# Kernel tuning notes

Hardware: AMD Instinct MI355X
Metric: run time of the kernel (lower is better)

The kernel has to match this reference:

```python
import jax, jax.numpy as jnp
import numpy as np

OUT_F, IN_F, BLOCK, RANK = 8192, 8192, 32, 16
B, S = 4, 256
Q_ZERO = 128.0      # symmetric int8-style zero point for the Q8_0-like quants
LORA_SCALE = 2.0    # patch alpha applied by the patch function


def setup_inputs() -> dict:
    key = jax.random.key(0)
    k1, k2, k3, k4, k5, k6 = jax.random.split(key, 6)
    x = jax.random.normal(k1, (B, S, IN_F), dtype=jnp.float32)
    # block-quantized weight: int quants in [0,256) and per-block scales
    q_int = jax.random.randint(k2, (OUT_F, IN_F // BLOCK, BLOCK), 0, 256, dtype=jnp.int32)
    scales = jax.random.uniform(k3, (OUT_F, IN_F // BLOCK), dtype=jnp.float32) * 0.02
    lora_A = jax.random.normal(k4, (RANK, IN_F), dtype=jnp.float32) * 0.02
    lora_B = jax.random.normal(k5, (OUT_F, RANK), dtype=jnp.float32) * 0.02
    bias = jax.random.normal(k6, (OUT_F,), dtype=jnp.float32)
    return {"x": x, "q_int": q_int, "scales": scales,
            "lora_A": lora_A, "lora_B": lora_B, "bias": bias}


def reference(x, q_int, scales, lora_A, lora_B, bias):
    # --- get_weight(): dequantize GGML block-quantized tensor ---
    # w[o, b, e] = (q[o, b, e] - 128) * scale[o, b]
    w = (q_int.astype(jnp.float32) - Q_ZERO) * scales[:, :, None]   # [out, in//BLOCK, BLOCK]
    w = w.reshape(OUT_F, IN_F)                                      # [out, in]
    # --- apply patch function (LoRA add) ---
    w = w + LORA_SCALE * (lora_B @ lora_A)                          # [out, in]
    # --- cast_bias_weight + F.linear ---
    w = w.astype(x.dtype)
    y = jnp.einsum('bsi,oi->bso', x, w) + bias.astype(x.dtype)      # [B, S, out]
    return y
```

## Files before the change

### kernel.cpp

```cpp
#include <hip/hip_runtime.h>
#include <hip/hip_bf16.h>
#include <stdint.h>

#define OUT_F 8192
#define IN_F  8192
#define RANK  16
#define M_TOT 1024
#define BM 128
#define BN 128
#define BK 64
#define WP 72

typedef __bf16 bf16x8 __attribute__((ext_vector_type(8)));
typedef float  f32x4  __attribute__((ext_vector_type(4)));

static __device__ __forceinline__ uint32_t pack_bf16(float lo, float hi) {
    uint32_t a = __builtin_bit_cast(uint32_t, lo);
    uint32_t b = __builtin_bit_cast(uint32_t, hi);
    return ((a + 0x8000u) >> 16) | ((b + 0x8000u) & 0xffff0000u);
}

__global__ __launch_bounds__(256) void prep_kernel(
    const float* __restrict__ x, const float* __restrict__ lora_A,
    uint2* __restrict__ xb2, float* __restrict__ t)
{
    const int m   = blockIdx.x;
    const int tid = threadIdx.x;
    const float4* x4 = (const float4*)(x + (size_t)m * IN_F);
    uint2* xout = xb2 + (size_t)m * (IN_F / 4);

    float acc[RANK];
#pragma unroll
    for (int r = 0; r < RANK; ++r) acc[r] = 0.f;

#pragma unroll
    for (int j = 0; j < 8; ++j) {
        const int idx4 = tid + 256 * j;
        const float4 v = x4[idx4];
        uint2 p;
        p.x = pack_bf16(v.x, v.y);
        p.y = pack_bf16(v.z, v.w);
        xout[idx4] = p;
        const int i = idx4 * 4;
#pragma unroll
        for (int r = 0; r < RANK; ++r) {
            const float4 a = *(const float4*)(lora_A + (size_t)r * IN_F + i);
            acc[r] += v.x * a.x + v.y * a.y + v.z * a.z + v.w * a.w;
        }
    }
#pragma unroll
    for (int r = 0; r < RANK; ++r) {
        float v = acc[r];
        for (int off = 32; off > 0; off >>= 1) v += __shfl_down(v, off, 64);
        acc[r] = v;
    }
    __shared__ float part[4][RANK];
    const int wave = tid >> 6, lane = tid & 63;
    if (lane == 0) {
#pragma unroll
        for (int r = 0; r < RANK; ++r) part[wave][r] = acc[r];
    }
    __syncthreads();
    if (tid < RANK)
        t[(size_t)m * RANK + tid] = part[0][tid] + part[1][tid] + part[2][tid] + part[3][tid];
}

__global__ __launch_bounds__(256, 2) void gemm_kernel(
    const uint16_t* __restrict__ xb,
    const int*      __restrict__ q,
    const float*    __restrict__ scales,
    const float*    __restrict__ t,
    const float*    __restrict__ loraB,
    const float*    __restrict__ bias,
    float*          __restrict__ out)
{
    __shared__ __align__(16) uint16_t xs[BM * BK];
    __shared__ __align__(16) uint16_t wt[BN * WP];

    const int bx    = blockIdx.x;
    const int mtile = bx >> 6;
    const int ntile = bx & 63;
    const int m0 = mtile * BM;
    const int n0 = ntile * BN;

    const int tid  = threadIdx.x;
    const int wave = tid >> 6;
    const int lane = tid & 63;
    const int wm = wave & 1, wn = wave >> 1;
    const int fr = lane & 15;
    const int fk = (lane >> 4) * 8;
    const int quad = lane >> 4;

    const int qrow_base = tid >> 4;
    const int qcol4     = (tid & 15) * 4;
    const int qhi       = (tid >> 3) & 1;

    f32x4 acc[4][4];
    const f32x4 z = {0.f, 0.f, 0.f, 0.f};
#pragma unroll
    for (int i = 0; i < 4; ++i)
#pragma unroll
        for (int j = 0; j < 4; ++j) acc[i][j] = z;

    {
        if (tid < 128) {
            const int row = tid;
            const float4* tp = (const float4*)(t + (size_t)(m0 + row) * RANK);
            const float4 v0 = tp[0], v1 = tp[1], v2 = tp[2], v3 = tp[3];
            uint32_t* dst = (uint32_t*)(xs + row * BK);
            dst[0] = pack_bf16(v0.x, v0.y); dst[1] = pack_bf16(v0.z, v0.w);
            dst[2] = pack_bf16(v1.x, v1.y); dst[3] = pack_bf16(v1.z, v1.w);
            dst[4] = pack_bf16(v2.x, v2.y); dst[5] = pack_bf16(v2.z, v2.w);
            dst[6] = pack_bf16(v3.x, v3.y); dst[7] = pack_bf16(v3.z, v3.w);
#pragma unroll
            for (int i = 8; i < 16; ++i) dst[i] = 0;
        } else {
            const int row = tid - 128;
            const float4* bp = (const float4*)(loraB + (size_t)(n0 + row) * RANK);
            const float4 v0 = bp[0], v1 = bp[1], v2 = bp[2], v3 = bp[3];
            uint32_t* dst = (uint32_t*)(wt + row * WP);
            dst[0] = pack_bf16(2.f * v0.x, 2.f * v0.y); dst[1] = pack_bf16(2.f * v0.z, 2.f * v0.w);
            dst[2] = pack_bf16(2.f * v1.x, 2.f * v1.y); dst[3] = pack_bf16(2.f * v1.z, 2.f * v1.w);
            dst[4] = pack_bf16(2.f * v2.x, 2.f * v2.y); dst[5] = pack_bf16(2.f * v2.z, 2.f * v2.w);
            dst[6] = pack_bf16(2.f * v3.x, 2.f * v3.y); dst[7] = pack_bf16(2.f * v3.z, 2.f * v3.w);
#pragma unroll
            for (int i = 8; i < 16; ++i) dst[i] = 0;
        }
        __syncthreads();
        bf16x8 af[4], bfr[4];
#pragma unroll
        for (int i = 0; i < 4; ++i)
            af[i] = *(const bf16x8*)(xs + (wm * 64 + i * 16 + fr) * BK + fk);
#pragma unroll
        for (int j = 0; j < 4; ++j)
            bfr[j] = *(const bf16x8*)(wt + (wn * 64 + j * 16 + fr) * WP + fk);
#pragma unroll
        for (int i = 0; i < 4; ++i)
#pragma unroll
            for (int j = 0; j < 4; ++j)
                acc[i][j] = __builtin_amdgcn_mfma_f32_16x16x32_bf16(af[i], bfr[j], acc[i][j], 0, 0, 0);
    }

    const int* qbase = q + (size_t)n0 * IN_F + qcol4;
    const uint16_t* xsrc = xb + (size_t)(m0 + wave * 32 + (lane >> 3)) * IN_F + (lane & 7) * 8;

    for (int kt = 0; kt < IN_F / BK; ++kt) {
        __syncthreads();

        {
            const uint16_t* g = xsrc + kt * BK;
#pragma unroll
            for (int i = 0; i < 4; ++i) {
                __builtin_amdgcn_global_load_lds(
                    (const __attribute__((address_space(1))) uint32_t*)(g + (size_t)i * 8 * IN_F),
                    (__attribute__((address_space(3))) uint32_t*)(xs + (wave * 32 + i * 8) * BK),
                    16, 0, 0);
            }
        }
        {
            int4  qv[8];
            float sc[8];
#pragma unroll
            for (int j = 0; j < 8; ++j) {
                const int row = qrow_base + 16 * j;
                qv[j] = *(const int4*)(qbase + (size_t)row * IN_F + kt * 64);
                sc[j] = scales[(size_t)(n0 + row) * (IN_F / 32) + kt * 2 + qhi];
            }
#pragma unroll
            for (int j = 0; j < 8; ++j) {
                const float s = sc[j];
                const float c = -128.f * s;
                const float f0 = fmaf((float)qv[j].x, s, c);
                const float f1 = fmaf((float)qv[j].y, s, c);
                const float f2 = fmaf((float)qv[j].z, s, c);
                const float f3 = fmaf((float)qv[j].w, s, c);
                uint2 p;
                p.x = pack_bf16(f0, f1);
                p.y = pack_bf16(f2, f3);
                const int row = qrow_base + 16 * j;
                *(uint2*)(wt + row * WP + qcol4) = p;
            }
        }
        __syncthreads();

#pragma unroll
        for (int kk = 0; kk < BK; kk += 32) {
            bf16x8 af[4], bfr[4];
#pragma unroll
            for (int i = 0; i < 4; ++i)
                af[i] = *(const bf16x8*)(xs + (wm * 64 + i * 16 + fr) * BK + kk + fk);
#pragma unroll
            for (int j = 0; j < 4; ++j)
                bfr[j] = *(const bf16x8*)(wt + (wn * 64 + j * 16 + fr) * WP + kk + fk);
#pragma unroll
            for (int i = 0; i < 4; ++i)
#pragma unroll
                for (int j = 0; j < 4; ++j)
                    acc[i][j] = __builtin_amdgcn_mfma_f32_16x16x32_bf16(af[i], bfr[j], acc[i][j], 0, 0, 0);
        }
    }

#pragma unroll
    for (int j = 0; j < 4; ++j) {
        const int col = n0 + wn * 64 + j * 16 + fr;
        const float bv = bias[col];
#pragma unroll
        for (int i = 0; i < 4; ++i) {
            const int rbase = m0 + wm * 64 + i * 16 + quad * 4;
#pragma unroll
            for (int r = 0; r < 4; ++r)
                out[(size_t)(rbase + r) * OUT_F + col] = acc[i][j][r] + bv;
        }
    }
}

extern "C" void kernel_launch(void* const* d_in, const int* in_sizes, int n_in,
                              void* d_out, int out_size, void* d_ws, size_t ws_size,
                              hipStream_t stream) {
    const float* x      = (const float*)d_in[0];
    const int*   q      = (const int*)d_in[1];
    const float* scales = (const float*)d_in[2];
    const float* lora_A = (const float*)d_in[3];
    const float* lora_B = (const float*)d_in[4];
    const float* bias   = (const float*)d_in[5];
    float* out = (float*)d_out;

    uint16_t* xb = (uint16_t*)d_ws;
    float*    t  = (float*)((char*)d_ws + (size_t)M_TOT * IN_F * sizeof(uint16_t));

    prep_kernel<<<M_TOT, 256, 0, stream>>>(x, lora_A, (uint2*)xb, t);
    gemm_kernel<<<(M_TOT / BM) * (OUT_F / BN), 256, 0, stream>>>(
        xb, q, scales, t, lora_B, bias, out);
}
```

Measured before the change: 657.3 us.

## Shrink N tile, prefetch quants across iterations, swizzle LDS, MFMA LoRA projection

Halves the GEMM N tile to 64 and raises the occupancy hint so more blocks fit per CU. The int32 quant and scale loads for the next K step are now issued after the barrier, so they overlap the current MFMA work. The x tile in LDS gets an XOR swizzle to cut bank conflicts. The prep kernel is split into a flat bf16 convert kernel and a separate MFMA-based x·A^T kernel that accumulates with atomics. In exchange, the x tile is reloaded twice as often per output, and the LoRA projection now rounds to bf16 and depends on atomic accumulation order.

```diff
diff --git a/kernel.cpp b/kernel.cpp
--- a/kernel.cpp
+++ b/kernel.cpp
@@ -7,9 +7,10 @@
 #define RANK  16
 #define M_TOT 1024
 #define BM 128
-#define BN 128
+#define BN 64
 #define BK 64
 #define WP 72
+#define NK (IN_F / BK)
 
 typedef __bf16 bf16x8 __attribute__((ext_vector_type(8)));
 typedef float  f32x4  __attribute__((ext_vector_type(4)));
@@ -20,52 +21,61 @@
     return ((a + 0x8000u) >> 16) | ((b + 0x8000u) & 0xffff0000u);
 }
 
-__global__ __launch_bounds__(256) void prep_kernel(
-    const float* __restrict__ x, const float* __restrict__ lora_A,
-    uint2* __restrict__ xb2, float* __restrict__ t)
+__global__ __launch_bounds__(256) void convert_kernel(
+    const float* __restrict__ x, uint2* __restrict__ xb2, float* __restrict__ t)
 {
-    const int m   = blockIdx.x;
-    const int tid = threadIdx.x;
-    const float4* x4 = (const float4*)(x + (size_t)m * IN_F);
-    uint2* xout = xb2 + (size_t)m * (IN_F / 4);
-
-    float acc[RANK];
-#pragma unroll
-    for (int r = 0; r < RANK; ++r) acc[r] = 0.f;
-
+    const int tid = threadIdx.x, b = blockIdx.x;
+    if (b < 64) t[b * 256 + tid] = 0.f;
+    const float4* x4 = (const float4*)x;
+    const int base = b * 256 + tid;
 #pragma unroll
     for (int j = 0; j < 8; ++j) {
-        const int idx4 = tid + 256 * j;
-        const float4 v = x4[idx4];
+        const int i = base + j * 262144;
+        const float4 v = x4[i];
         uint2 p;
         p.x = pack_bf16(v.x, v.y);
         p.y = pack_bf16(v.z, v.w);
-        xout[idx4] = p;
-        const int i = idx4 * 4;
-#pragma unroll
-        for (int r = 0; r < RANK; ++r) {
-            const float4 a = *(const float4*)(lora_A + (size_t)r * IN_F + i);
-            acc[r] += v.x * a.x + v.y * a.y + v.z * a.z + v.w * a.w;
-        }
-    }
-#pragma unroll
-    for (int r = 0; r < RANK; ++r) {
-        float v = acc[r];
-        for (int off = 32; off > 0; off >>= 1) v += __shfl_down(v, off, 64);
-        acc[r] = v;
-    }
-    __shared__ float part[4][RANK];
-    const int wave = tid >> 6, lane = tid & 63;
-    if (lane == 0) {
-#pragma unroll
-        for (int r = 0; r < RANK; ++r) part[wave][r] = acc[r];
-    }
-    __syncthreads();
-    if (tid < RANK)
-        t[(size_t)m * RANK + tid] = part[0][tid] + part[1][tid] + part[2][tid] + part[3][tid];
-}
-
-__global__ __launch_bounds__(256, 2) void gemm_kernel(
+        xb2[i] = p;
+    }
+}
+
+__global__ __launch_bounds__(256) void lora_t_kernel(
+    const float* __restrict__ x, const float* __restrict__ lora_A,
+    float* __restrict__ t)
+{
+    const int b = blockIdx.x;
+    const int mt = b >> 4, ks = b & 15;
+    const int tid = threadIdx.x, wave = tid >> 6, lane = tid & 63;
+    const int fr = lane & 15, quad = lane >> 4;
+    const int m = mt * 64 + wave * 16 + fr;
+    const int k0 = ks * 512 + quad * 8;
+
+    f32x4 acc = {0.f, 0.f, 0.f, 0.f};
+    const float* xr = x + (size_t)m * IN_F + k0;
+    const float* ar = lora_A + (size_t)fr * IN_F + k0;
+
+#pragma unroll 4
+    for (int s = 0; s < 16; ++s) {
+        const float4 x0 = *(const float4*)(xr + s * 32);
+        const float4 x1 = *(const float4*)(xr + s * 32 + 4);
+        const float4 a0 = *(const float4*)(ar + s * 32);
+        const float4 a1 = *(const float4*)(ar + s * 32 + 4);
+        bf16x8 af, bfr;
+        uint32_t* ap = (uint32_t*)&af;
+        uint32_t* bp = (uint32_t*)&bfr;
+        ap[0] = pack_bf16(x0.x, x0.y); ap[1] = pack_bf16(x0.z, x0.w);
+        ap[2] = pack_bf16(x1.x, x1.y); ap[3] = pack_bf16(x1.z, x1.w);
+        bp[0] = pack_bf16(a0.x, a0.y); bp[1] = pack_bf16(a0.z, a0.w);
+        bp[2] = pack_bf16(a1.x, a1.y); bp[3] = pack_bf16(a1.z, a1.w);
+        acc = __builtin_amdgcn_mfma_f32_16x16x32_bf16(af, bfr, acc, 0, 0, 0);
+    }
+    const int mout = mt * 64 + wave * 16 + quad * 4;
+#pragma unroll
+    for (int r = 0; r < 4; ++r)
+        atomicAdd(&t[(size_t)(mout + r) * RANK + fr], acc[r]);
+}
+
+__global__ __launch_bounds__(256, 4) void gemm_kernel(
     const uint16_t* __restrict__ xb,
     const int*      __restrict__ q,
     const float*    __restrict__ scales,
@@ -78,8 +88,8 @@
     __shared__ __align__(16) uint16_t wt[BN * WP];
 
     const int bx    = blockIdx.x;
-    const int mtile = bx >> 6;
-    const int ntile = bx & 63;
+    const int mtile = bx >> 7;
+    const int ntile = bx & 127;
     const int m0 = mtile * BM;
     const int n0 = ntile * BN;
 
@@ -88,33 +98,53 @@
     const int lane = tid & 63;
     const int wm = wave & 1, wn = wave >> 1;
     const int fr = lane & 15;
-    const int fk = (lane >> 4) * 8;
     const int quad = lane >> 4;
-
-    const int qrow_base = tid >> 4;
-    const int qcol4     = (tid & 15) * 4;
-    const int qhi       = (tid >> 3) & 1;
-
-    f32x4 acc[4][4];
+    const int fk = quad * 8;
+
+    const int qrow  = tid >> 4;
+    const int qcol4 = (tid & 15) * 4;
+    const int qhi   = (tid >> 3) & 1;
+
+    f32x4 acc[4][2];
     const f32x4 z = {0.f, 0.f, 0.f, 0.f};
 #pragma unroll
     for (int i = 0; i < 4; ++i)
 #pragma unroll
-        for (int j = 0; j < 4; ++j) acc[i][j] = z;
+        for (int j = 0; j < 2; ++j) acc[i][j] = z;
+
+    const int* qbase = q + (size_t)n0 * IN_F + qcol4;
+    int4  qv[4];
+    float sc[4];
+#pragma unroll
+    for (int j = 0; j < 4; ++j) {
+        const int row = qrow + 16 * j;
+        qv[j] = *(const int4*)(qbase + (size_t)row * IN_F);
+        sc[j] = scales[(size_t)(n0 + row) * (IN_F / 32) + qhi];
+    }
 
     {
         if (tid < 128) {
             const int row = tid;
+            const int s = row & 7;
             const float4* tp = (const float4*)(t + (size_t)(m0 + row) * RANK);
             const float4 v0 = tp[0], v1 = tp[1], v2 = tp[2], v3 = tp[3];
+            uint32_t vals[8];
+            vals[0] = pack_bf16(v0.x, v0.y); vals[1] = pack_bf16(v0.z, v0.w);
+            vals[2] = pack_bf16(v1.x, v1.y); vals[3] = pack_bf16(v1.z, v1.w);
+            vals[4] = pack_bf16(v2.x, v2.y); vals[5] = pack_bf16(v2.z, v2.w);
+            vals[6] = pack_bf16(v3.x, v3.y); vals[7] = pack_bf16(v3.z, v3.w);
             uint32_t* dst = (uint32_t*)(xs + row * BK);
-            dst[0] = pack_bf16(v0.x, v0.y); dst[1] = pack_bf16(v0.z, v0.w);
-            dst[2] = pack_bf16(v1.x, v1.y); dst[3] = pack_bf16(v1.z, v1.w);
-            dst[4] = pack_bf16(v2.x, v2.y); dst[5] = pack_bf16(v2.z, v2.w);
-            dst[6] = pack_bf16(v3.x, v3.y); dst[7] = pack_bf16(v3.z, v3.w);
-#pragma unroll
-            for (int i = 8; i < 16; ++i) dst[i] = 0;
-        } else {
+#pragma unroll
+            for (int c = 0; c < 8; ++c) {
+                const int p = (c ^ s) * 4;
+                if (c < 2) {
+                    dst[p + 0] = vals[c * 4 + 0]; dst[p + 1] = vals[c * 4 + 1];
+                    dst[p + 2] = vals[c * 4 + 2]; dst[p + 3] = vals[c * 4 + 3];
+                } else {
+                    dst[p + 0] = 0; dst[p + 1] = 0; dst[p + 2] = 0; dst[p + 3] = 0;
+                }
+            }
+        } else if (tid < 192) {
             const int row = tid - 128;
             const float4* bp = (const float4*)(loraB + (size_t)(n0 + row) * RANK);
             const float4 v0 = bp[0], v1 = bp[1], v2 = bp[2], v3 = bp[3];
@@ -127,82 +157,85 @@
             for (int i = 8; i < 16; ++i) dst[i] = 0;
         }
         __syncthreads();
-        bf16x8 af[4], bfr[4];
+        bf16x8 af[4], bfr[2];
+#pragma unroll
+        for (int i = 0; i < 4; ++i) {
+            const int R = wm * 64 + i * 16 + fr;
+            const int p = (quad ^ (fr & 7)) * 8;
+            af[i] = *(const bf16x8*)(xs + R * BK + p);
+        }
+#pragma unroll
+        for (int j = 0; j < 2; ++j)
+            bfr[j] = *(const bf16x8*)(wt + (wn * 32 + j * 16 + fr) * WP + fk);
 #pragma unroll
         for (int i = 0; i < 4; ++i)
-            af[i] = *(const bf16x8*)(xs + (wm * 64 + i * 16 + fr) * BK + fk);
-#pragma unroll
-        for (int j = 0; j < 4; ++j)
-            bfr[j] = *(const bf16x8*)(wt + (wn * 64 + j * 16 + fr) * WP + fk);
-#pragma unroll
-        for (int i = 0; i < 4; ++i)
-#pragma unroll
-            for (int j = 0; j < 4; ++j)
+#pragma unroll
+            for (int j = 0; j < 2; ++j)
                 acc[i][j] = __builtin_amdgcn_mfma_f32_16x16x32_bf16(af[i], bfr[j], acc[i][j], 0, 0, 0);
     }
 
-    const int* qbase = q + (size_t)n0 * IN_F + qcol4;
-    const uint16_t* xsrc = xb + (size_t)(m0 + wave * 32 + (lane >> 3)) * IN_F + (lane & 7) * 8;
-
-    for (int kt = 0; kt < IN_F / BK; ++kt) {
+    const int xrow   = wave * 32 + (lane >> 3);
+    const int xchunk = (lane & 7) ^ (lane >> 3);
+    const uint16_t* xsrc = xb + (size_t)(m0 + xrow) * IN_F + xchunk * 8;
+
+    for (int kt = 0; kt < NK; ++kt) {
         __syncthreads();
 
+#pragma unroll
+        for (int i = 0; i < 4; ++i) {
+            __builtin_amdgcn_global_load_lds(
+                (const __attribute__((address_space(1))) uint32_t*)(xsrc + kt * BK + (size_t)i * 8 * IN_F),
+                (__attribute__((address_space(3))) uint32_t*)(xs + (wave * 32 + i * 8) * BK),
+                16, 0, 0);
+        }
+#pragma unroll
+        for (int j = 0; j < 4; ++j) {
+            const float s = sc[j];
+            const float c = -128.f * s;
+            const float f0 = fmaf((float)qv[j].x, s, c);
+            const float f1 = fmaf((float)qv[j].y, s, c);
+            const float f2 = fmaf((float)qv[j].z, s, c);
+            const float f3 = fmaf((float)qv[j].w, s, c);
+            uint2 p;
+            p.x = pack_bf16(f0, f1);
+            p.y = pack_bf16(f2, f3);
+            *(uint2*)(wt + (qrow + 16 * j) * WP + qcol4) = p;
+        }
+        __syncthreads();
+
         {
-            const uint16_t* g = xsrc + kt * BK;
+            const int ktn = (kt + 1) & (NK - 1);
+#pragma unroll
+            for (int j = 0; j < 4; ++j) {
+                const int row = qrow + 16 * j;
+                qv[j] = *(const int4*)(qbase + (size_t)row * IN_F + ktn * BK);
+                sc[j] = scales[(size_t)(n0 + row) * (IN_F / 32) + ktn * 2 + qhi];
+            }
+        }
+
+#pragma unroll
+        for (int kk = 0; kk < BK; kk += 32) {
+            bf16x8 af[4], bfr[2];
 #pragma unroll
             for (int i = 0; i < 4; ++i) {
-                __builtin_amdgcn_global_load_lds(
-                    (const __attribute__((address_space(1))) uint32_t*)(g + (size_t)i * 8 * IN_F),
-                    (__attribute__((address_space(3))) uint32_t*)(xs + (wave * 32 + i * 8) * BK),
-                    16, 0, 0);
+                const int R = wm * 64 + i * 16 + fr;
+                const int p = (((kk >> 3) + quad) ^ (fr & 7)) * 8;
+                af[i] = *(const bf16x8*)(xs + R * BK + p);
             }
-        }
-        {
-            int4  qv[8];
-            float sc[8];
-#pragma unroll
-            for (int j = 0; j < 8; ++j) {
-                const int row = qrow_base + 16 * j;
-                qv[j] = *(const int4*)(qbase + (size_t)row * IN_F + kt * 64);
-                sc[j] = scales[(size_t)(n0 + row) * (IN_F / 32) + kt * 2 + qhi];
-            }
-#pragma unroll
-            for (int j = 0; j < 8; ++j) {
-                const float s = sc[j];
-                const float c = -128.f * s;
-                const float f0 = fmaf((float)qv[j].x, s, c);
-                const float f1 = fmaf((float)qv[j].y, s, c);
-                const float f2 = fmaf((float)qv[j].z, s, c);
-                const float f3 = fmaf((float)qv[j].w, s, c);
-                uint2 p;
-                p.x = pack_bf16(f0, f1);
-                p.y = pack_bf16(f2, f3);
-                const int row = qrow_base + 16 * j;
-                *(uint2*)(wt + row * WP + qcol4) = p;
-            }
-        }
-        __syncthreads();
-
-#pragma unroll
-        for (int kk = 0; kk < BK; kk += 32) {
-            bf16x8 af[4], bfr[4];
+#pragma unroll
+            for (int j = 0; j < 2; ++j)
+                bfr[j] = *(const bf16x8*)(wt + (wn * 32 + j * 16 + fr) * WP + kk + fk);
 #pragma unroll
             for (int i = 0; i < 4; ++i)
-                af[i] = *(const bf16x8*)(xs + (wm * 64 + i * 16 + fr) * BK + kk + fk);
-#pragma unroll
-            for (int j = 0; j < 4; ++j)
-                bfr[j] = *(const bf16x8*)(wt + (wn * 64 + j * 16 + fr) * WP + kk + fk);
-#pragma unroll
-            for (int i = 0; i < 4; ++i)
-#pragma unroll
-                for (int j = 0; j < 4; ++j)
+#pragma unroll
+                for (int j = 0; j < 2; ++j)
                     acc[i][j] = __builtin_amdgcn_mfma_f32_16x16x32_bf16(af[i], bfr[j], acc[i][j], 0, 0, 0);
         }
     }
 
 #pragma unroll
-    for (int j = 0; j < 4; ++j) {
-        const int col = n0 + wn * 64 + j * 16 + fr;
+    for (int j = 0; j < 2; ++j) {
+        const int col = n0 + wn * 32 + j * 16 + fr;
         const float bv = bias[col];
 #pragma unroll
         for (int i = 0; i < 4; ++i) {
@@ -228,7 +261,8 @@
     uint16_t* xb = (uint16_t*)d_ws;
     float*    t  = (float*)((char*)d_ws + (size_t)M_TOT * IN_F * sizeof(uint16_t));
 
-    prep_kernel<<<M_TOT, 256, 0, stream>>>(x, lora_A, (uint2*)xb, t);
+    convert_kernel<<<M_TOT, 256, 0, stream>>>(x, (uint2*)xb, t);
+    lora_t_kernel<<<256, 256, 0, stream>>>(x, lora_A, t);
     gemm_kernel<<<(M_TOT / BM) * (OUT_F / BN), 256, 0, stream>>>(
         xb, q, scales, t, lora_B, bias, out);
 }
```

Result: faster. 624.6 us (-5.0%).
